# Optimization experiments

Hardware: AMD Instinct MI355X
Metric: run time of the kernel (lower is better)

## Reference

```python
import jax, jax.numpy as jnp
import numpy as np

N, E, F_IN, H = 50000, 800000, 2, 128
S, G = 5000, 64  # num subgraphs, num graphs (static segment counts)
N_EXTRA_CONVS = 3  # num_layers - 1


def setup_inputs() -> dict:
    key = jax.random.key(0)
    ks = jax.random.split(key, 16)
    inv = lambda f: 1.0 / np.sqrt(f)
    return {
        "x": jax.random.normal(ks[0], (N, F_IN), dtype=jnp.float32),
        "edge_index": jax.random.randint(ks[1], (2, E), 0, N),
        "node_to_subgraph": jax.random.randint(ks[2], (N,), 0, S),
        "subgraph_to_graph": jax.random.randint(ks[3], (S,), 0, G),
        "W1a": jax.random.normal(ks[4], (F_IN, H), dtype=jnp.float32) * inv(F_IN),
        "b1a": jnp.zeros((H,), jnp.float32),
        "W1b": jax.random.normal(ks[5], (H, H), dtype=jnp.float32) * inv(H),
        "b1b": jnp.zeros((H,), jnp.float32),
        "convs_Wa": jax.random.normal(ks[6], (N_EXTRA_CONVS, H, H), dtype=jnp.float32) * inv(H),
        "convs_ba": jnp.zeros((N_EXTRA_CONVS, H), jnp.float32),
        "convs_Wb": jax.random.normal(ks[7], (N_EXTRA_CONVS, H, H), dtype=jnp.float32) * inv(H),
        "convs_bb": jnp.zeros((N_EXTRA_CONVS, H), jnp.float32),
        "lin1_W": jax.random.normal(ks[8], (H, H), dtype=jnp.float32) * inv(H),
        "lin1_b": jnp.zeros((H,), jnp.float32),
        "lin2_W": jax.random.normal(ks[9], (H, H), dtype=jnp.float32) * inv(H),
        "lin2_b": jnp.zeros((H,), jnp.float32),
    }


def reference(x, edge_index, node_to_subgraph, subgraph_to_graph,
              W1a, b1a, W1b, b1b, convs_Wa, convs_ba, convs_Wb, convs_bb,
              lin1_W, lin1_b, lin2_W, lin2_b):
    src, dst = edge_index[0], edge_index[1]

    def gin_conv(h, Wa, ba, Wb, bb):
        # GIN aggregation (eps=0): h_i + sum over incoming neighbors
        aggr = jax.ops.segment_sum(h[src], dst, num_segments=N)
        h = h + aggr
        h = jax.nn.relu(h @ Wa + ba)
        return jax.nn.relu(h @ Wb + bb)

    h = gin_conv(x, W1a, b1a, W1b, b1b)
    for i in range(N_EXTRA_CONVS):
        h = gin_conv(h, convs_Wa[i], convs_ba[i], convs_Wb[i], convs_bb[i])

    # nested pooling: nodes -> subgraphs -> graphs
    h = jax.ops.segment_sum(h, node_to_subgraph, num_segments=S)
    h = jax.ops.segment_sum(h, subgraph_to_graph, num_segments=G)

    h = jax.nn.relu(h @ lin1_W + lin1_b)
    # dropout is identity in eval mode
    h = h @ lin2_W + lin2_b
    return jax.nn.log_softmax(h, axis=1)
```

## Files before the change

### kernel.cpp

```cpp
#include <hip/hip_runtime.h>
#include <cstddef>

#define N_NODES  50000
#define N_EDGES  800000
#define HDIM     128
#define SSUB     5000
#define GGRAPH   64
#define FILL_Q   416
#define PB       (8 * FILL_Q)
#define LDSW     136

#define NB 196
#define SB 20
#define WB 448

typedef unsigned int uint;
typedef unsigned short ushort;
typedef __attribute__((ext_vector_type(8))) short bf16x8;
typedef __attribute__((ext_vector_type(16))) float f32x16;

__device__ __forceinline__ float bflo(uint v) { return __uint_as_float(v << 16); }
__device__ __forceinline__ float bfhi(uint v) { return __uint_as_float(v & 0xffff0000u); }
__device__ __forceinline__ uint packbf(float lo, float hi) {
    uint a = __float_as_uint(lo), b = __float_as_uint(hi);
    a = (a + 0x7fff + ((a >> 16) & 1)) >> 16;
    b = (b + 0x7fff + ((b >> 16) & 1)) & 0xffff0000u;
    return a | b;
}
__device__ __forceinline__ ushort bf16of(float f) {
    uint a = __float_as_uint(f);
    a = (a + 0x7fff + ((a >> 16) & 1)) >> 16;
    return (ushort)a;
}


__global__ __launch_bounds__(256) void k_prep(const int* __restrict__ src,
                                              const int* __restrict__ dst,
                                              int* __restrict__ deg,
                                              int* __restrict__ csrcF,
                                              const int* __restrict__ n2s,
                                              int* __restrict__ sdeg,
                                              int* __restrict__ s2nF,
                                              const int* __restrict__ s2g,
                                              int* __restrict__ gcnt,
                                              int* __restrict__ g2sF,
                                              const float* __restrict__ W1b,
                                              const float* __restrict__ cWa,
                                              const float* __restrict__ cWb,
                                              ushort* __restrict__ wt) {
    int b = blockIdx.x, t = threadIdx.x;
    if (b < PB) {
        int part = b & 7;
        int q = b >> 3;
        int lo = part * 6250, hi = lo + 6250;
        for (int e = q * 256 + t; e < N_EDGES; e += FILL_Q * 256) {
            int d = dst[e];
            if (d >= lo && d < hi) {
                int pos = atomicAdd(&deg[d], 1);
                if (pos < 64) csrcF[(d << 6) + pos] = src[e];
            }
        }
    } else if (b < PB + NB) {
        int i = (b - PB) * 256 + t;
        if (i < N_NODES) {
            int sg = n2s[i];
            int pos = atomicAdd(&sdeg[sg], 1);
            if (pos < 32) s2nF[(sg << 5) + pos] = i;
        }
    } else if (b < PB + NB + SB) {
        int i = (b - PB - NB) * 256 + t;
        if (i < SSUB) {
            int g = s2g[i];
            int pos = atomicAdd(&gcnt[g], 1);
            if (pos < 128) g2sF[(g << 7) + pos] = i;
        }
    } else {
        int gid = (b - PB - NB - SB) * 256 + t;
        int m = gid >> 14, r = gid & 16383;
        int n = r >> 7, k = r & 127;
        const float* Wsrc = (m == 0) ? W1b
                          : (m <= 3) ? cWa + (size_t)(m - 1) * 16384
                                     : cWb + (size_t)(m - 4) * 16384;
        wt[gid] = bf16of(Wsrc[k * 128 + n]);
    }
}


__global__ __launch_bounds__(256) void k_layer1(const float2* __restrict__ x,
                                                const int* __restrict__ deg,
                                                const int* __restrict__ csrcF,
                                                const float* __restrict__ W1a,
                                                const float* __restrict__ b1a,
                                                const ushort* __restrict__ WtA,
                                                const float* __restrict__ bA,
                                                ushort* __restrict__ hbout) {
    __shared__ ushort lds[64 * LDSW];
    __shared__ float2 sums[64];
    const int tid = threadIdx.x, wave = tid >> 6, lane = tid & 63;
    const int nodeBase = blockIdx.x * 64;

    {
        int nl = tid >> 2, sub = tid & 3;
        int gn = nodeBase + nl;
        float tx = 0.f, ty = 0.f;
        if (gn < N_NODES) {
            int e = deg[gn]; if (e > 64) e = 64;
            for (int k = sub; k < e; k += 4) {
                float2 v = x[csrcF[(gn << 6) + k]];
                tx += v.x; ty += v.y;
            }
        }
        tx += __shfl_xor(tx, 1); ty += __shfl_xor(ty, 1);
        tx += __shfl_xor(tx, 2); ty += __shfl_xor(ty, 2);
        if (sub == 0) {
            if (gn < N_NODES) {
                float2 sv = x[gn];
                sums[nl] = make_float2(tx + sv.x, ty + sv.y);
            } else {
                sums[nl] = make_float2(0.f, 0.f);
            }
        }
    }
    __syncthreads();

    {
        float2 wlo = ((const float2*)W1a)[lane];
        float2 whi = ((const float2*)W1a)[64 + lane];
        float2 bv  = ((const float2*)b1a)[lane];
        for (int n = wave * 16; n < wave * 16 + 16; ++n) {
            float2 ts = sums[n];
            float v0 = fmaf(ts.x, wlo.x, fmaf(ts.y, whi.x, bv.x));
            float v1 = fmaf(ts.x, wlo.y, fmaf(ts.y, whi.y, bv.y));
            *(uint*)(&lds[n * LDSW + 2 * lane]) = packbf(fmaxf(v0, 0.f), fmaxf(v1, 0.f));
        }
    }

    const int l32 = lane & 31, hk = lane >> 5;
    const int colBase = wave * 32;
    bf16x8 wa[8];
#pragma unroll
    for (int kk = 0; kk < 8; ++kk)
        wa[kk] = *(const bf16x8*)(WtA + (size_t)(colBase + l32) * 128 + kk * 16 + hk * 8);
    const float biasA = bA[colBase + l32];
    __syncthreads();

    f32x16 acc[2];
#pragma unroll
    for (int m = 0; m < 2; ++m)
#pragma unroll
        for (int r = 0; r < 16; ++r) acc[m][r] = 0.f;
#pragma unroll
    for (int m = 0; m < 2; ++m) {
        const ushort* arow = lds + (m * 32 + l32) * LDSW + hk * 8;
#pragma unroll
        for (int kk = 0; kk < 8; ++kk) {
            bf16x8 a = *(const bf16x8*)(arow + kk * 16);
            acc[m] = __builtin_amdgcn_mfma_f32_32x32x16_bf16(a, wa[kk], acc[m], 0, 0, 0);
        }
    }

#pragma unroll
    for (int m = 0; m < 2; ++m) {
#pragma unroll
        for (int r = 0; r < 16; ++r) {
            int rl = (r & 3) + 8 * (r >> 2) + 4 * hk;
            int row = nodeBase + m * 32 + rl;
            if (row < N_NODES)
                hbout[(size_t)row * 128 + colBase + l32] =
                    bf16of(fmaxf(acc[m][r] + biasA, 0.f));
        }
    }
}


__global__ __launch_bounds__(256) void k_aggr128_bf16(const uint* __restrict__ hb,
                                                      const int* __restrict__ deg,
                                                      const int* __restrict__ csrcF,
                                                      uint* __restrict__ out) {
    int node = blockIdx.x * 4 + (threadIdx.x >> 6);
    int lane = threadIdx.x & 63;
    int cnt = deg[node]; if (cnt > 64) cnt = 64;
    uint sv = hb[(size_t)node * 64 + lane];
    float ax0 = bflo(sv), ay0 = bfhi(sv);
    float ax1 = 0.f, ay1 = 0.f, ax2 = 0.f, ay2 = 0.f, ax3 = 0.f, ay3 = 0.f;
    int idx = csrcF[(node << 6) + ((lane < cnt) ? lane : 0)];
    int j = 0;
    for (; j + 15 < cnt; j += 16) {
        int s0 = __shfl(idx, j),      s1 = __shfl(idx, j + 1);
        int s2 = __shfl(idx, j + 2),  s3 = __shfl(idx, j + 3);
        int s4 = __shfl(idx, j + 4),  s5 = __shfl(idx, j + 5);
        int s6 = __shfl(idx, j + 6),  s7 = __shfl(idx, j + 7);
        int s8 = __shfl(idx, j + 8),  s9 = __shfl(idx, j + 9);
        int sa = __shfl(idx, j + 10), sb = __shfl(idx, j + 11);
        int sc = __shfl(idx, j + 12), sd = __shfl(idx, j + 13);
        int se = __shfl(idx, j + 14), sf = __shfl(idx, j + 15);
        uint v0 = hb[(size_t)s0 * 64 + lane];
        uint v1 = hb[(size_t)s1 * 64 + lane];
        uint v2 = hb[(size_t)s2 * 64 + lane];
        uint v3 = hb[(size_t)s3 * 64 + lane];
        uint v4 = hb[(size_t)s4 * 64 + lane];
        uint v5 = hb[(size_t)s5 * 64 + lane];
        uint v6 = hb[(size_t)s6 * 64 + lane];
        uint v7 = hb[(size_t)s7 * 64 + lane];
        uint v8 = hb[(size_t)s8 * 64 + lane];
        uint v9 = hb[(size_t)s9 * 64 + lane];
        uint va = hb[(size_t)sa * 64 + lane];
        uint vb = hb[(size_t)sb * 64 + lane];
        uint vc = hb[(size_t)sc * 64 + lane];
        uint vd = hb[(size_t)sd * 64 + lane];
        uint ve = hb[(size_t)se * 64 + lane];
        uint vf = hb[(size_t)sf * 64 + lane];
        ax0 += bflo(v0); ay0 += bfhi(v0);
        ax1 += bflo(v1); ay1 += bfhi(v1);
        ax2 += bflo(v2); ay2 += bfhi(v2);
        ax3 += bflo(v3); ay3 += bfhi(v3);
        ax0 += bflo(v4); ay0 += bfhi(v4);
        ax1 += bflo(v5); ay1 += bfhi(v5);
        ax2 += bflo(v6); ay2 += bfhi(v6);
        ax3 += bflo(v7); ay3 += bfhi(v7);
        ax0 += bflo(v8); ay0 += bfhi(v8);
        ax1 += bflo(v9); ay1 += bfhi(v9);
        ax2 += bflo(va); ay2 += bfhi(va);
        ax3 += bflo(vb); ay3 += bfhi(vb);
        ax0 += bflo(vc); ay0 += bfhi(vc);
        ax1 += bflo(vd); ay1 += bfhi(vd);
        ax2 += bflo(ve); ay2 += bfhi(ve);
        ax3 += bflo(vf); ay3 += bfhi(vf);
    }
    for (; j + 3 < cnt; j += 4) {
        int s0 = __shfl(idx, j),     s1 = __shfl(idx, j + 1);
        int s2 = __shfl(idx, j + 2), s3 = __shfl(idx, j + 3);
        uint v0 = hb[(size_t)s0 * 64 + lane];
        uint v1 = hb[(size_t)s1 * 64 + lane];
        uint v2 = hb[(size_t)s2 * 64 + lane];
        uint v3 = hb[(size_t)s3 * 64 + lane];
        ax0 += bflo(v0); ay0 += bfhi(v0);
        ax1 += bflo(v1); ay1 += bfhi(v1);
        ax2 += bflo(v2); ay2 += bfhi(v2);
        ax3 += bflo(v3); ay3 += bfhi(v3);
    }
    for (; j < cnt; ++j) {
        int sj = __shfl(idx, j);
        uint v = hb[(size_t)sj * 64 + lane];
        ax0 += bflo(v); ay0 += bfhi(v);
    }
    out[(size_t)node * 64 + lane] =
        packbf((ax0 + ax1) + (ax2 + ax3), (ay0 + ay1) + (ay2 + ay3));
}


__global__ __launch_bounds__(256) void k_mlp(const ushort* __restrict__ A,
                                             const ushort* __restrict__ WtA,
                                             const float* __restrict__ bA,
                                             const ushort* __restrict__ WtB,
                                             const float* __restrict__ bB,
                                             ushort* __restrict__ C, int nrows) {
    __shared__ ushort ldsA[64 * LDSW];
    __shared__ ushort ldsB[64 * LDSW];
    const int tid = threadIdx.x;
    const int wave = tid >> 6, lane = tid & 63;
    const int l32 = lane & 31, hk = lane >> 5;
    const int colBase = wave * 32;
    const int rowBase = blockIdx.x * 64;

    {
        int r = tid >> 2;
        int qo = (tid & 3) * 32;
        const uint4* gp = (const uint4*)(A + (size_t)(rowBase + r) * 128 + qo);
        uint4* lp = (uint4*)(ldsA + r * LDSW + qo);
        bool valid = (rowBase + r) < nrows;
#pragma unroll
        for (int q = 0; q < 4; ++q) {
            uint4 v = valid ? gp[q] : (uint4){0u, 0u, 0u, 0u};
            lp[q] = v;
        }
    }

    bf16x8 wa[8], wb[8];
#pragma unroll
    for (int kk = 0; kk < 8; ++kk) {
        wa[kk] = *(const bf16x8*)(WtA + (size_t)(colBase + l32) * 128 + kk * 16 + hk * 8);
        wb[kk] = *(const bf16x8*)(WtB + (size_t)(colBase + l32) * 128 + kk * 16 + hk * 8);
    }
    const float biasA = bA[colBase + l32];
    const float biasB = bB[colBase + l32];
    __syncthreads();

    f32x16 acc[2];
#pragma unroll
    for (int m = 0; m < 2; ++m)
#pragma unroll
        for (int r = 0; r < 16; ++r) acc[m][r] = 0.f;
#pragma unroll
    for (int m = 0; m < 2; ++m) {
        const ushort* arow = ldsA + (m * 32 + l32) * LDSW + hk * 8;
#pragma unroll
        for (int kk = 0; kk < 8; ++kk) {
            bf16x8 a = *(const bf16x8*)(arow + kk * 16);
            acc[m] = __builtin_amdgcn_mfma_f32_32x32x16_bf16(a, wa[kk], acc[m], 0, 0, 0);
        }
    }

#pragma unroll
    for (int m = 0; m < 2; ++m) {
#pragma unroll
        for (int r = 0; r < 16; ++r) {
            int rl = (r & 3) + 8 * (r >> 2) + 4 * hk;
            ldsB[(m * 32 + rl) * LDSW + colBase + l32] =
                bf16of(fmaxf(acc[m][r] + biasA, 0.f));
        }
    }
    __syncthreads();

#pragma unroll
    for (int m = 0; m < 2; ++m)
#pragma unroll
        for (int r = 0; r < 16; ++r) acc[m][r] = 0.f;
#pragma unroll
    for (int m = 0; m < 2; ++m) {
        const ushort* arow = ldsB + (m * 32 + l32) * LDSW + hk * 8;
#pragma unroll
        for (int kk = 0; kk < 8; ++kk) {
            bf16x8 a = *(const bf16x8*)(arow + kk * 16);
            acc[m] = __builtin_amdgcn_mfma_f32_32x32x16_bf16(a, wb[kk], acc[m], 0, 0, 0);
        }
    }

#pragma unroll
    for (int m = 0; m < 2; ++m) {
#pragma unroll
        for (int r = 0; r < 16; ++r) {
            int rl = (r & 3) + 8 * (r >> 2) + 4 * hk;
            int row = rowBase + m * 32 + rl;
            if (row < nrows)
                C[(size_t)row * 128 + colBase + l32] =
                    bf16of(fmaxf(acc[m][r] + biasB, 0.f));
        }
    }
}


__global__ __launch_bounds__(1024) void k_poolfinal(const uint* __restrict__ hb,
                                                    const int* __restrict__ sdeg,
                                                    const int* __restrict__ s2nF,
                                                    const int* __restrict__ gcnt,
                                                    const int* __restrict__ g2sF,
                                                    const float* __restrict__ W1,
                                                    const float* __restrict__ b1,
                                                    const float* __restrict__ W2,
                                                    const float* __restrict__ b2,
                                                    float* __restrict__ out) {
    __shared__ float gacc[16][130];
    __shared__ float row[128];
    __shared__ float t1[128];
    __shared__ float red[128];
    const int g = blockIdx.x;
    const int tid = threadIdx.x;
    const int wave = tid >> 6, lane = tid & 63;

    int ns = gcnt[g]; if (ns > 128) ns = 128;
    float ax = 0.f, ay = 0.f;
    for (int si = wave; si < ns; si += 16) {
        int sg = g2sF[(g << 7) + si];
        int ec = sdeg[sg]; if (ec > 32) ec = 32;
        int idx = s2nF[(sg << 5) + ((lane < ec) ? lane : 0)];
        int j = 0;
        for (; j + 3 < ec; j += 4) {
            int n0 = __shfl(idx, j),     n1 = __shfl(idx, j + 1);
            int n2 = __shfl(idx, j + 2), n3 = __shfl(idx, j + 3);
            uint v0 = hb[(size_t)n0 * 64 + lane];
            uint v1 = hb[(size_t)n1 * 64 + lane];
            uint v2 = hb[(size_t)n2 * 64 + lane];
            uint v3 = hb[(size_t)n3 * 64 + lane];
            ax += bflo(v0) + bflo(v1) + bflo(v2) + bflo(v3);
            ay += bfhi(v0) + bfhi(v1) + bfhi(v2) + bfhi(v3);
        }
        for (; j < ec; ++j) {
            int nj = __shfl(idx, j);
            uint v = hb[(size_t)nj * 64 + lane];
            ax += bflo(v); ay += bfhi(v);
        }
    }
    gacc[wave][2 * lane]     = ax;
    gacc[wave][2 * lane + 1] = ay;
    __syncthreads();

    if (tid < 128) {
        float s = 0.f;
#pragma unroll
        for (int w = 0; w < 16; ++w) s += gacc[w][tid];
        row[tid] = s;
    }
    __syncthreads();

    float s2 = 0.f;
    if (tid < 128) {
        float s1 = b1[tid];
        for (int k = 0; k < 128; ++k) s1 = fmaf(row[k], W1[k * 128 + tid], s1);
        t1[tid] = fmaxf(s1, 0.f);
    }
    __syncthreads();
    if (tid < 128) {
        s2 = b2[tid];
        for (int k = 0; k < 128; ++k) s2 = fmaf(t1[k], W2[k * 128 + tid], s2);
        red[tid] = s2;
    }
    __syncthreads();
    for (int off = 64; off > 0; off >>= 1) {
        if (tid < off) red[tid] = fmaxf(red[tid], red[tid + off]);
        __syncthreads();
    }
    float m = red[0];
    __syncthreads();
    if (tid < 128) red[tid] = expf(s2 - m);
    __syncthreads();
    for (int off = 64; off > 0; off >>= 1) {
        if (tid < off) red[tid] += red[tid + off];
        __syncthreads();
    }
    if (tid < 128) out[g * 128 + tid] = s2 - (m + logf(red[0]));
}


extern "C" void kernel_launch(void* const* d_in, const int* in_sizes, int n_in,
                              void* d_out, int out_size, void* d_ws, size_t ws_size,
                              hipStream_t stream) {
    (void)in_sizes; (void)n_in; (void)out_size; (void)ws_size;
    const float* x    = (const float*)d_in[0];
    const int*   ei   = (const int*)d_in[1];
    const int*   n2s  = (const int*)d_in[2];
    const int*   s2g  = (const int*)d_in[3];
    const float* W1a  = (const float*)d_in[4];
    const float* b1a  = (const float*)d_in[5];
    const float* W1b  = (const float*)d_in[6];
    const float* b1b  = (const float*)d_in[7];
    const float* cWa  = (const float*)d_in[8];
    const float* cba  = (const float*)d_in[9];
    const float* cWb  = (const float*)d_in[10];
    const float* cbb  = (const float*)d_in[11];
    const float* l1W  = (const float*)d_in[12];
    const float* l1b  = (const float*)d_in[13];
    const float* l2W  = (const float*)d_in[14];
    const float* l2b  = (const float*)d_in[15];
    float* out = (float*)d_out;

    uint*  hb    = (uint*)d_ws;
    uint*  habuf = hb + (size_t)N_NODES * 64;
    int*   csrcF = (int*)(habuf + (size_t)N_NODES * 64);
    int*   s2nF  = csrcF + (size_t)N_NODES * 64;
    int*   g2sF  = s2nF + SSUB * 32;
    int*   deg   = g2sF + GGRAPH * 128;
    int*   sdeg  = deg + N_NODES;
    int*   gcnt  = sdeg + SSUB;
    ushort* wt   = (ushort*)(gcnt + GGRAPH);

    const int* srcA = ei;
    const int* dstA = ei + N_EDGES;
    const int nTileBlocks = (N_NODES + 63) / 64;

    hipMemsetAsync(deg, 0, (size_t)(N_NODES + SSUB + GGRAPH) * 4, stream);

    k_prep<<<PB + NB + SB + WB, 256, 0, stream>>>(srcA, dstA, deg, csrcF,
                                                  n2s, sdeg, s2nF,
                                                  s2g, gcnt, g2sF,
                                                  W1b, cWa, cWb, wt);

    k_layer1<<<nTileBlocks, 256, 0, stream>>>((const float2*)x, deg, csrcF,
                                              W1a, b1a, wt, b1b, (ushort*)hb);

    for (int i = 0; i < 3; ++i) {
        k_aggr128_bf16<<<N_NODES / 4, 256, 0, stream>>>(hb, deg, csrcF, habuf);
        k_mlp<<<nTileBlocks, 256, 0, stream>>>((const ushort*)habuf,
                                               wt + (size_t)(1 + i) * 16384,
                                               cba + i * HDIM,
                                               wt + (size_t)(4 + i) * 16384,
                                               cbb + i * HDIM,
                                               (ushort*)hb, N_NODES);
    }

    k_poolfinal<<<GGRAPH, 1024, 0, stream>>>(hb, sdeg, s2nF, gcnt, g2sF,
                                             l1W, l1b, l2W, l2b, out);
}
```

Baseline: 313.4 us.

## Partition edge fill by hardware XCD with per-XCD dynamic chunk counters

The CSR fill blocks no longer take their destination partition from the block index. Each block reads its XCC id from a hardware register and handles the destination range assigned to that XCD. Work comes in 2048-edge chunks claimed from a per-XCD atomic counter, so atomics on deg and the csrcF writes for a range stay within one XCD's L2, and load balances dynamically. The cost is extra block-level syncs, counter atomics, and a dependence on how the hardware places blocks across XCDs; every XCD still scans the full dst array.

```diff
diff --git a/kernel.cpp b/kernel.cpp
--- a/kernel.cpp
+++ b/kernel.cpp
@@ -6,8 +6,9 @@
 #define HDIM     128
 #define SSUB     5000
 #define GGRAPH   64
-#define FILL_Q   416
-#define PB       (8 * FILL_Q)
+#define PB       3328
+#define CHUNK    2048
+#define NCHUNK   ((N_EDGES + CHUNK - 1) / CHUNK)
 #define LDSW     136
 
 #define NB 196
@@ -38,6 +39,7 @@
                                               const int* __restrict__ dst,
                                               int* __restrict__ deg,
                                               int* __restrict__ csrcF,
+                                              int* __restrict__ chunkCtr,
                                               const int* __restrict__ n2s,
                                               int* __restrict__ sdeg,
                                               int* __restrict__ s2nF,
@@ -50,15 +52,32 @@
                                               ushort* __restrict__ wt) {
     int b = blockIdx.x, t = threadIdx.x;
     if (b < PB) {
-        int part = b & 7;
-        int q = b >> 3;
-        int lo = part * 6250, hi = lo + 6250;
-        for (int e = q * 256 + t; e < N_EDGES; e += FILL_Q * 256) {
-            int d = dst[e];
-            if (d >= lo && d < hi) {
-                int pos = atomicAdd(&deg[d], 1);
-                if (pos < 64) csrcF[(d << 6) + pos] = src[e];
+        uint xcd;
+        asm volatile("s_getreg_b32 %0, hwreg(HW_REG_XCC_ID, 0, 4)" : "=s"(xcd));
+        xcd &= 7;
+        const int lo = (int)xcd * 6250, hi = lo + 6250;
+        for (;;) {
+            int c;
+            if (t == 0) c = atomicAdd(&chunkCtr[xcd], 1);
+            c = __shfl(c, 0);
+            __shared__ int csh;
+            if (t == 0) csh = c;
+            __syncthreads();
+            c = csh;
+            if (c >= NCHUNK) break;
+            int base = c * CHUNK;
+#pragma unroll
+            for (int i = 0; i < CHUNK / 256; ++i) {
+                int e = base + i * 256 + t;
+                if (e < N_EDGES) {
+                    int d = dst[e];
+                    if (d >= lo && d < hi) {
+                        int pos = atomicAdd(&deg[d], 1);
+                        if (pos < 64) csrcF[(d << 6) + pos] = src[e];
+                    }
+                }
             }
+            __syncthreads();
         }
     } else if (b < PB + NB) {
         int i = (b - PB) * 256 + t;
@@ -444,23 +463,24 @@
     const float* l2b  = (const float*)d_in[15];
     float* out = (float*)d_out;
 
-    uint*  hb    = (uint*)d_ws;
-    uint*  habuf = hb + (size_t)N_NODES * 64;
-    int*   csrcF = (int*)(habuf + (size_t)N_NODES * 64);
-    int*   s2nF  = csrcF + (size_t)N_NODES * 64;
-    int*   g2sF  = s2nF + SSUB * 32;
-    int*   deg   = g2sF + GGRAPH * 128;
-    int*   sdeg  = deg + N_NODES;
-    int*   gcnt  = sdeg + SSUB;
-    ushort* wt   = (ushort*)(gcnt + GGRAPH);
+    uint*  hb      = (uint*)d_ws;
+    uint*  habuf   = hb + (size_t)N_NODES * 64;
+    int*   csrcF   = (int*)(habuf + (size_t)N_NODES * 64);
+    int*   s2nF    = csrcF + (size_t)N_NODES * 64;
+    int*   g2sF    = s2nF + SSUB * 32;
+    int*   deg     = g2sF + GGRAPH * 128;
+    int*   sdeg    = deg + N_NODES;
+    int*   gcnt    = sdeg + SSUB;
+    int*   chunkCtr= gcnt + GGRAPH;
+    ushort* wt     = (ushort*)(chunkCtr + 8);
 
     const int* srcA = ei;
     const int* dstA = ei + N_EDGES;
     const int nTileBlocks = (N_NODES + 63) / 64;
 
-    hipMemsetAsync(deg, 0, (size_t)(N_NODES + SSUB + GGRAPH) * 4, stream);
-
-    k_prep<<<PB + NB + SB + WB, 256, 0, stream>>>(srcA, dstA, deg, csrcF,
+    hipMemsetAsync(deg, 0, (size_t)(N_NODES + SSUB + GGRAPH + 8) * 4, stream);
+
+    k_prep<<<PB + NB + SB + WB, 256, 0, stream>>>(srcA, dstA, deg, csrcF, chunkCtr,
                                                   n2s, sdeg, s2nF,
                                                   s2g, gcnt, g2sF,
                                                   W1b, cWa, cWb, wt);
```

New measurement: 370.6 us. 1.18x slower.
